# Kernel tuning notes

Measured on AMD Instinct MI355X. Metric: run time of the kernel, lower is better.

## Reference

```python
import jax, jax.numpy as jnp
import numpy as np


def setup_inputs() -> dict:
    key = jax.random.key(0)
    k1, k2, k3 = jax.random.split(key, 3)
    B, C, P = 16384, 2048, 256
    f_struct = jax.random.normal(k1, (B, C), dtype=jnp.float32)
    pids = jax.random.randint(k2, (B,), 0, P, dtype=jnp.int64)
    camids = jax.random.randint(k3, (B,), 0, 2, dtype=jnp.int64)
    return {"f_struct": f_struct, "pids": pids, "camids": camids, "num_pids": P}


def reference(f_struct, pids, camids, num_pids):
    # Fused segment reduction over joint (pid, camid) groups: seg = pid*2 + camid
    seg = (pids * 2 + camids).astype(jnp.int32)
    n_seg = num_pids * 2
    sums = jax.ops.segment_sum(f_struct, seg, num_segments=n_seg)          # [2P, C]
    counts = jax.ops.segment_sum(jnp.ones_like(seg, dtype=f_struct.dtype),
                                 seg, num_segments=n_seg)                   # [2P]
    means = sums / jnp.maximum(counts, 1)[:, None]                          # safe mean
    means = means.reshape(num_pids, 2, -1)                                  # [P, 2, C]
    counts = counts.reshape(num_pids, 2)                                    # [P, 2]
    # per-pid MSE between visible (cam 0) and thermal (cam 1) centers
    diff = means[:, 0, :] - means[:, 1, :]
    mse = jnp.mean(diff * diff, axis=-1)                                    # [P]
    valid = (counts[:, 0] > 0) & (counts[:, 1] > 0)                         # [P]
    cnt = jnp.sum(valid.astype(f_struct.dtype))
    loss = jnp.sum(jnp.where(valid, mse, 0.0)) / jnp.maximum(cnt, 1)
    return jnp.where(cnt > 0, loss, jnp.zeros((), dtype=f_struct.dtype))
```

## Files before the change

kernel.cpp:

```cpp
#include <hip/hip_runtime.h>

#define NPID 256
#define CC   2048
#define CCH  (CC / 2)
#define TPB  1024
#define CAP  512
#define PIPE 8

__device__ __forceinline__ float2 seg_stream(const float2* __restrict__ f2,
                                             const int* __restrict__ list,
                                             int c, int t)
{
    float2 acc = make_float2(0.f, 0.f);
    if (c <= 0) return acc;

    float2 buf[PIPE];
#pragma unroll
    for (int k = 0; k < PIPE; ++k) {
        int idx = (k < c) ? k : (c - 1);
        int r = __builtin_amdgcn_readfirstlane(list[idx]);
        buf[k] = f2[(size_t)r * CCH + t];
    }
    __builtin_amdgcn_sched_barrier(0);

    int i = 0;
    for (; i + PIPE <= c; ) {
        float2 cur[PIPE];
#pragma unroll
        for (int k = 0; k < PIPE; ++k) cur[k] = buf[k];
        i += PIPE;
#pragma unroll
        for (int k = 0; k < PIPE; ++k) {
            int idx = (i + k < c) ? (i + k) : (c - 1);
            int r = __builtin_amdgcn_readfirstlane(list[idx]);
            buf[k] = f2[(size_t)r * CCH + t];
        }
        __builtin_amdgcn_sched_barrier(0);
#pragma unroll
        for (int k = 0; k < PIPE; ++k) { acc.x += cur[k].x; acc.y += cur[k].y; }
    }
#pragma unroll
    for (int k = 0; k < PIPE; ++k) {
        if (i + k < c) { acc.x += buf[k].x; acc.y += buf[k].y; }
    }
    return acc;
}

__global__ __launch_bounds__(TPB) void main_k(
    const float* __restrict__ f, const int* __restrict__ pids,
    const int* __restrict__ camids, float* __restrict__ mse,
    float* __restrict__ valid, int B)
{
    __shared__ int list0[CAP], list1[CAP];
    __shared__ int cnt0_s, cnt1_s;

    const int p = blockIdx.x;
    const int t = threadIdx.x;

    if (t == 0) { cnt0_s = 0; cnt1_s = 0; }
    __syncthreads();

    const int4* p4 = reinterpret_cast<const int4*>(pids);
    const int4* c4 = reinterpret_cast<const int4*>(camids);
    const int nv = B >> 2;
    for (int i = t; i < nv; i += TPB) {
        int4 pv = p4[i];
        int4 cv = c4[i];
        int base = i << 2;
        if (pv.x == p) { int pos = atomicAdd(cv.x ? &cnt1_s : &cnt0_s, 1);
                         if (pos < CAP) (cv.x ? list1 : list0)[pos] = base; }
        if (pv.y == p) { int pos = atomicAdd(cv.y ? &cnt1_s : &cnt0_s, 1);
                         if (pos < CAP) (cv.y ? list1 : list0)[pos] = base + 1; }
        if (pv.z == p) { int pos = atomicAdd(cv.z ? &cnt1_s : &cnt0_s, 1);
                         if (pos < CAP) (cv.z ? list1 : list0)[pos] = base + 2; }
        if (pv.w == p) { int pos = atomicAdd(cv.w ? &cnt1_s : &cnt0_s, 1);
                         if (pos < CAP) (cv.w ? list1 : list0)[pos] = base + 3; }
    }
    __syncthreads();
    const int c0 = min(cnt0_s, CAP), c1 = min(cnt1_s, CAP);

    const float2* f2 = reinterpret_cast<const float2*>(f);
    float2 a0 = seg_stream(f2, list0, c0, t);
    float2 a1 = seg_stream(f2, list1, c1, t);

    const float i0 = 1.0f / (float)(c0 > 0 ? c0 : 1);
    const float i1 = 1.0f / (float)(c1 > 0 ? c1 : 1);
    const float dx = a0.x * i0 - a1.x * i1;
    const float dy = a0.y * i0 - a1.y * i1;
    float sq = dx * dx + dy * dy;

    for (int off = 32; off; off >>= 1) sq += __shfl_down(sq, off);
    __shared__ float wred[TPB / 64];
    if ((t & 63) == 0) wred[t >> 6] = sq;
    __syncthreads();
    if (t == 0) {
        float tot = 0.f;
#pragma unroll
        for (int w = 0; w < TPB / 64; ++w) tot += wred[w];
        mse[p]   = tot;
        valid[p] = (c0 > 0 && c1 > 0) ? 1.0f : 0.0f;
    }
}

__global__ __launch_bounds__(256) void reduce_k(
    const float* __restrict__ mse, const float* __restrict__ valid,
    float* __restrict__ out)
{
    int t = threadIdx.x;
    float v   = valid[t];
    float num = v * mse[t] * (1.0f / (float)CC);
    float cv  = v;
    for (int off = 32; off; off >>= 1) {
        num += __shfl_down(num, off);
        cv  += __shfl_down(cv, off);
    }
    __shared__ float nred[4], cred[4];
    if ((t & 63) == 0) { nred[t >> 6] = num; cred[t >> 6] = cv; }
    __syncthreads();
    if (t == 0) {
        float N  = nred[0] + nred[1] + nred[2] + nred[3];
        float Cv = cred[0] + cred[1] + cred[2] + cred[3];
        out[0] = (Cv > 0.0f) ? (N / fmaxf(Cv, 1.0f)) : 0.0f;
    }
}

extern "C" void kernel_launch(void* const* d_in, const int* in_sizes, int n_in,
                              void* d_out, int out_size, void* d_ws, size_t ws_size,
                              hipStream_t stream)
{
    const float* f      = (const float*)d_in[0];
    const int*   pids   = (const int*)d_in[1];
    const int*   camids = (const int*)d_in[2];

    int B = in_sizes[1];

    float* mse   = (float*)d_ws;
    float* valid = (float*)((char*)d_ws + 1024);

    main_k<<<NPID, TPB, 0, stream>>>(f, pids, camids, mse, valid, B);
    reduce_k<<<1, 256, 0, stream>>>(mse, valid, (float*)d_out);
}
```

Measured before the change: 202.9 us.

## Split rows into halves per pid, widen loads to float4, add partial-sum stage

Each pid is now handled by two blocks, each scanning half of the batch rows. The blocks write per-half partial sums and counts to workspace, and a new stage-2 kernel combines the halves and computes the MSE. Block size drops to 512 threads, feature loads widen to float4, and the prefetch pipeline deepens with interleaved accumulate-and-load. The aim is more concurrent blocks and memory-level parallelism on the gather, at the cost of an extra kernel launch and a partial-sum round trip through memory. CAP drops to 256 per half, which relies on the uniform pid distribution.

```diff
diff --git a/kernel.cpp b/kernel.cpp
--- a/kernel.cpp
+++ b/kernel.cpp
@@ -1,93 +1,123 @@
 #include <hip/hip_runtime.h>
 
-#define NPID 256
-#define CC   2048
-#define CCH  (CC / 2)
-#define TPB  1024
-#define CAP  512
-#define PIPE 8
+#define NPID  256
+#define CC    2048
+#define CF4   (CC / 4)
+#define TPB   512
+#define NHALF 2
+#define HROWS (16384 / NHALF)
+#define CAP   256
+#define PIPE  16
 
-__device__ __forceinline__ float2 seg_stream(const float2* __restrict__ f2,
-                                             const int* __restrict__ list,
-                                             int c, int t)
+
+__device__ __forceinline__ void stream_rows(const float4* __restrict__ f4,
+                                            const int* __restrict__ list,
+                                            int c, int t, float4& acc)
 {
-    float2 acc = make_float2(0.f, 0.f);
-    if (c <= 0) return acc;
-
-    float2 buf[PIPE];
+    if (c <= 0) return;
+    float4 buf[PIPE];
 #pragma unroll
     for (int k = 0; k < PIPE; ++k) {
         int idx = (k < c) ? k : (c - 1);
         int r = __builtin_amdgcn_readfirstlane(list[idx]);
-        buf[k] = f2[(size_t)r * CCH + t];
+        buf[k] = f4[(size_t)r * CF4 + t];
     }
     __builtin_amdgcn_sched_barrier(0);
 
     int i = 0;
-    for (; i + PIPE <= c; ) {
-        float2 cur[PIPE];
-#pragma unroll
-        for (int k = 0; k < PIPE; ++k) cur[k] = buf[k];
-        i += PIPE;
+    for (; i + PIPE < c; i += PIPE) {
 #pragma unroll
         for (int k = 0; k < PIPE; ++k) {
-            int idx = (i + k < c) ? (i + k) : (c - 1);
+            float4 v = buf[k];
+            acc.x += v.x; acc.y += v.y; acc.z += v.z; acc.w += v.w;
+            int nxt = i + PIPE + k;
+            int idx = (nxt < c) ? nxt : (c - 1);
             int r = __builtin_amdgcn_readfirstlane(list[idx]);
-            buf[k] = f2[(size_t)r * CCH + t];
+            buf[k] = f4[(size_t)r * CF4 + t];
         }
-        __builtin_amdgcn_sched_barrier(0);
-#pragma unroll
-        for (int k = 0; k < PIPE; ++k) { acc.x += cur[k].x; acc.y += cur[k].y; }
     }
 #pragma unroll
     for (int k = 0; k < PIPE; ++k) {
-        if (i + k < c) { acc.x += buf[k].x; acc.y += buf[k].y; }
+        if (k < c - i) {
+            acc.x += buf[k].x; acc.y += buf[k].y;
+            acc.z += buf[k].z; acc.w += buf[k].w;
+        }
     }
-    return acc;
 }
 
-__global__ __launch_bounds__(TPB) void main_k(
+__global__ __launch_bounds__(TPB, 4) void main_k(
     const float* __restrict__ f, const int* __restrict__ pids,
-    const int* __restrict__ camids, float* __restrict__ mse,
-    float* __restrict__ valid, int B)
+    const int* __restrict__ camids, float* __restrict__ part,
+    int* __restrict__ cnt_g)
 {
     __shared__ int list0[CAP], list1[CAP];
     __shared__ int cnt0_s, cnt1_s;
 
-    const int p = blockIdx.x;
+    const int p = blockIdx.x >> 1;
+    const int h = blockIdx.x & 1;
     const int t = threadIdx.x;
 
     if (t == 0) { cnt0_s = 0; cnt1_s = 0; }
     __syncthreads();
 
-    const int4* p4 = reinterpret_cast<const int4*>(pids);
-    const int4* c4 = reinterpret_cast<const int4*>(camids);
-    const int nv = B >> 2;
+    const int base_row = h * HROWS;
+    const int4* p4 = reinterpret_cast<const int4*>(pids) + base_row / 4;
+    const int4* c4 = reinterpret_cast<const int4*>(camids) + base_row / 4;
+    const int nv = HROWS / 4;
     for (int i = t; i < nv; i += TPB) {
         int4 pv = p4[i];
         int4 cv = c4[i];
-        int base = i << 2;
+        int br = base_row + (i << 2);
         if (pv.x == p) { int pos = atomicAdd(cv.x ? &cnt1_s : &cnt0_s, 1);
-                         if (pos < CAP) (cv.x ? list1 : list0)[pos] = base; }
+                         if (pos < CAP) (cv.x ? list1 : list0)[pos] = br; }
         if (pv.y == p) { int pos = atomicAdd(cv.y ? &cnt1_s : &cnt0_s, 1);
-                         if (pos < CAP) (cv.y ? list1 : list0)[pos] = base + 1; }
+                         if (pos < CAP) (cv.y ? list1 : list0)[pos] = br + 1; }
         if (pv.z == p) { int pos = atomicAdd(cv.z ? &cnt1_s : &cnt0_s, 1);
-                         if (pos < CAP) (cv.z ? list1 : list0)[pos] = base + 2; }
+                         if (pos < CAP) (cv.z ? list1 : list0)[pos] = br + 2; }
         if (pv.w == p) { int pos = atomicAdd(cv.w ? &cnt1_s : &cnt0_s, 1);
-                         if (pos < CAP) (cv.w ? list1 : list0)[pos] = base + 3; }
+                         if (pos < CAP) (cv.w ? list1 : list0)[pos] = br + 3; }
     }
     __syncthreads();
     const int c0 = min(cnt0_s, CAP), c1 = min(cnt1_s, CAP);
 
-    const float2* f2 = reinterpret_cast<const float2*>(f);
-    float2 a0 = seg_stream(f2, list0, c0, t);
-    float2 a1 = seg_stream(f2, list1, c1, t);
+    const float4* f4 = reinterpret_cast<const float4*>(f);
+    float4 a0 = make_float4(0.f, 0.f, 0.f, 0.f);
+    float4 a1 = make_float4(0.f, 0.f, 0.f, 0.f);
+    stream_rows(f4, list0, c0, t, a0);
+    stream_rows(f4, list1, c1, t, a1);
+
+    float4* part4 = reinterpret_cast<float4*>(part);
+    part4[(size_t)(((2 * p + 0) * 2 + h)) * CF4 + t] = a0;
+    part4[(size_t)(((2 * p + 1) * 2 + h)) * CF4 + t] = a1;
+    if (t == 0) {
+        cnt_g[(2 * p + 0) * 2 + h] = c0;
+        cnt_g[(2 * p + 1) * 2 + h] = c1;
+    }
+}
+
+__global__ __launch_bounds__(TPB) void stage2_k(
+    const float* __restrict__ part, const int* __restrict__ cnt_g,
+    float* __restrict__ mse, float* __restrict__ valid)
+{
+    const int p = blockIdx.x;
+    const int t = threadIdx.x;
+    const float4* part4 = reinterpret_cast<const float4*>(part);
+
+    const int c0 = cnt_g[4 * p + 0] + cnt_g[4 * p + 1];
+    const int c1 = cnt_g[4 * p + 2] + cnt_g[4 * p + 3];
+
+    float4 s0a = part4[(size_t)(4 * p + 0) * CF4 + t];
+    float4 s0b = part4[(size_t)(4 * p + 1) * CF4 + t];
+    float4 s1a = part4[(size_t)(4 * p + 2) * CF4 + t];
+    float4 s1b = part4[(size_t)(4 * p + 3) * CF4 + t];
 
     const float i0 = 1.0f / (float)(c0 > 0 ? c0 : 1);
     const float i1 = 1.0f / (float)(c1 > 0 ? c1 : 1);
-    const float dx = a0.x * i0 - a1.x * i1;
-    const float dy = a0.y * i0 - a1.y * i1;
-    float sq = dx * dx + dy * dy;
+    float dx = (s0a.x + s0b.x) * i0 - (s1a.x + s1b.x) * i1;
+    float dy = (s0a.y + s0b.y) * i0 - (s1a.y + s1b.y) * i1;
+    float dz = (s0a.z + s0b.z) * i0 - (s1a.z + s1b.z) * i1;
+    float dw = (s0a.w + s0b.w) * i0 - (s1a.w + s1b.w) * i1;
+    float sq = dx * dx + dy * dy + dz * dz + dw * dw;
 
     for (int off = 32; off; off >>= 1) sq += __shfl_down(sq, off);
     __shared__ float wred[TPB / 64];
@@ -97,7 +127,7 @@
         float tot = 0.f;
 #pragma unroll
         for (int w = 0; w < TPB / 64; ++w) tot += wred[w];
-        mse[p]   = tot;
+        mse[p]   = tot * (1.0f / (float)CC);
         valid[p] = (c0 > 0 && c1 > 0) ? 1.0f : 0.0f;
     }
 }
@@ -108,7 +138,7 @@
 {
     int t = threadIdx.x;
     float v   = valid[t];
-    float num = v * mse[t] * (1.0f / (float)CC);
+    float num = v * mse[t];
     float cv  = v;
     for (int off = 32; off; off >>= 1) {
         num += __shfl_down(num, off);
@@ -132,11 +162,14 @@
     const int*   pids   = (const int*)d_in[1];
     const int*   camids = (const int*)d_in[2];
 
-    int B = in_sizes[1];
+    const size_t PART_BYTES = (size_t)1024 * CC * 4;
 
-    float* mse   = (float*)d_ws;
-    float* valid = (float*)((char*)d_ws + 1024);
+    float* part  = (float*)d_ws;
+    int*   cnt   = (int*)((char*)d_ws + PART_BYTES);
+    float* mse   = (float*)((char*)d_ws + PART_BYTES + 4096);
+    float* valid = (float*)((char*)d_ws + PART_BYTES + 8192);
 
-    main_k<<<NPID, TPB, 0, stream>>>(f, pids, camids, mse, valid, B);
+    main_k<<<NPID * NHALF, TPB, 0, stream>>>(f, pids, camids, part, cnt);
+    stage2_k<<<NPID, TPB, 0, stream>>>(part, cnt, mse, valid);
     reduce_k<<<1, 256, 0, stream>>>(mse, valid, (float*)d_out);
 }
```

Result: no change. 205.6 us (+1.3%).
